# Kernel tuning notes

Hardware: AMD Instinct MI355X
Metric: run time of the kernel (lower is better)

The kernel has to match this reference:

```python
import jax, jax.numpy as jnp
import numpy as np

B = 1_000_000   # collocation points
N = 64          # layers[1]: number of tiny identity-init linear+activation layers
D = 3           # layers[0]: per-layer feature dim (rho, p, u columns)


def setup_inputs() -> dict:
    key = jax.random.key(0)
    k_x, k_w, k_cr, k_cp, k_cu = jax.random.split(key, 5)
    x = jax.random.normal(k_x, (B, D), dtype=jnp.float32)
    # Per-layer weights: identity init (as in the module) plus small noise so
    # the N layers are not all identical in the test harness.
    eye = jnp.eye(D, dtype=jnp.float32)
    W = eye[None, :, :] + 0.01 * jax.random.normal(k_w, (N, D, D), dtype=jnp.float32)
    b = jnp.zeros((N, D), dtype=jnp.float32)
    # Frozen output heads (Linear(N, 1, bias=False)), all initialized from c_initial.
    c_rho = jax.random.normal(k_cr, (1, N), dtype=jnp.float32)
    c_p = jax.random.normal(k_cp, (1, N), dtype=jnp.float32)
    c_u = jax.random.normal(k_cu, (1, N), dtype=jnp.float32)
    return {"x": x, "W": W, "b": b, "c_rho": c_rho, "c_p": c_p, "c_u": c_u}


def reference(x, W, b, c_rho, c_p, c_u):
    # Original loop: for i in range(N): u = act(Linear_i(x)); gather columns 0,1,2
    # and iteratively torch.cat them. Vectorized: one batched tiny GEMM over all
    # N layers, then slice the three channels.
    # x: [B, D]; W: [N, D, D]; b: [N, D] -> u: [B, N, D]
    u = jnp.tanh(jnp.einsum('bd,nkd->bnk', x, W) + b[None, :, :])
    u_rho = u[:, :, 0]   # [B, N]
    u_p = u[:, :, 1]
    u_u = u[:, :, 2]
    out_rho = u_rho @ c_rho.T   # [B, 1]
    out_p = u_p @ c_p.T
    out_u = u_u @ c_u.T
    return (out_rho, out_p, out_u)
```

## Files before the change

### kernel.cpp

```cpp
#include <hip/hip_runtime.h>


#define NN   64
#define RPT  4
#define BLK  256

__device__ __forceinline__ float fexp2(float x) {
#if __has_builtin(__builtin_amdgcn_exp2f)
    return __builtin_amdgcn_exp2f(x);
#else
    return exp2f(x);
#endif
}
__device__ __forceinline__ float frcp(float x) {
#if __has_builtin(__builtin_amdgcn_rcpf)
    return __builtin_amdgcn_rcpf(x);
#else
    return 1.0f / x;
#endif
}

__global__ __launch_bounds__(BLK) void fused_tanh_heads(
    const float* __restrict__ x,
    const float* __restrict__ W,
    const float* __restrict__ bias,
    const float* __restrict__ c_rho,
    const float* __restrict__ c_p,
    const float* __restrict__ c_u,
    float* __restrict__ out,
    int B)
{
    __shared__ float sc[NN * 16];
    const int t = threadIdx.x;
    #pragma unroll
    for (int k = 0; k < 4; ++k) {
        const int idx = t + BLK * k;
        const int n = idx >> 4;
        const int o = idx & 15;
        const float K = 2.8853900817779268f;
        float v;
        if (o < 9)       v = W[n * 9 + o] * K;
        else if (o < 12) v = bias[n * 3 + (o - 9)] * K;
        else if (o == 12) v = c_rho[n];
        else if (o == 13) v = c_p[n];
        else if (o == 14) v = c_u[n];
        else              v = 0.0f;
        sc[idx] = v;
    }
    __syncthreads();

    float C0 = c_rho[t & 63], C1 = c_p[t & 63], C2 = c_u[t & 63];
    #pragma unroll
    for (int o = 1; o < 64; o <<= 1) {
        C0 += __shfl_xor(C0, o);
        C1 += __shfl_xor(C1, o);
        C2 += __shfl_xor(C2, o);
    }

    const int base = blockIdx.x * (BLK * RPT) + t;

    int   rows[RPT];
    float xs[RPT][3];
    #pragma unroll
    for (int i = 0; i < RPT; ++i) {
        const int r = base + i * BLK;
        rows[i] = r;
        const bool ok = (r < B);
        xs[i][0] = ok ? x[r * 3 + 0] : 0.0f;
        xs[i][1] = ok ? x[r * 3 + 1] : 0.0f;
        xs[i][2] = ok ? x[r * 3 + 2] : 0.0f;
    }

    float acc[RPT][3];
    #pragma unroll
    for (int i = 0; i < RPT; ++i) { acc[i][0] = acc[i][1] = acc[i][2] = 0.0f; }

    const float4* q4 = (const float4*)sc;
    #pragma unroll 2
    for (int n = 0; n < NN; ++n) {
        const float4 q0 = q4[n * 4 + 0];
        const float4 q1 = q4[n * 4 + 1];
        const float4 q2 = q4[n * 4 + 2];
        const float4 q3 = q4[n * 4 + 3];
        #pragma unroll
        for (int i = 0; i < RPT; ++i) {
            const float x0 = xs[i][0], x1 = xs[i][1], x2 = xs[i][2];
            const float h0 = fmaf(x2, q0.z, fmaf(x1, q0.y, fmaf(x0, q0.x, q2.y)));
            const float h1 = fmaf(x2, q1.y, fmaf(x1, q1.x, fmaf(x0, q0.w, q2.z)));
            const float h2 = fmaf(x2, q2.x, fmaf(x1, q1.w, fmaf(x0, q1.z, q2.w)));
            const float a0 = fexp2(h0) + 1.0f;
            const float a1 = fexp2(h1) + 1.0f;
            const float a2 = fexp2(h2) + 1.0f;
            const float m  = a0 * a1;
            const float rr = frcp(m * a2);
            const float i2 = m  * rr;
            const float s  = a2 * rr;
            const float i0 = a1 * s;
            const float i1 = a0 * s;
            acc[i][0] = fmaf(i0, q3.x, acc[i][0]);
            acc[i][1] = fmaf(i1, q3.y, acc[i][1]);
            acc[i][2] = fmaf(i2, q3.z, acc[i][2]);
        }
    }

    #pragma unroll
    for (int i = 0; i < RPT; ++i) {
        const int r = rows[i];
        if (r < B) {
            out[r]         = fmaf(-2.0f, acc[i][0], C0);
            out[B + r]     = fmaf(-2.0f, acc[i][1], C1);
            out[2 * B + r] = fmaf(-2.0f, acc[i][2], C2);
        }
    }
}

extern "C" void kernel_launch(void* const* d_in, const int* in_sizes, int n_in,
                              void* d_out, int out_size, void* d_ws, size_t ws_size,
                              hipStream_t stream) {
    (void)d_ws; (void)ws_size; (void)n_in; (void)out_size;
    const float* x     = (const float*)d_in[0];
    const float* W     = (const float*)d_in[1];
    const float* bias  = (const float*)d_in[2];
    const float* c_rho = (const float*)d_in[3];
    const float* c_p   = (const float*)d_in[4];
    const float* c_u   = (const float*)d_in[5];
    float* out = (float*)d_out;

    const int B = in_sizes[0] / 3;
    const int rows_per_block = BLK * RPT;
    const int grid = (B + rows_per_block - 1) / rows_per_block;

    fused_tanh_heads<<<grid, BLK, 0, stream>>>(x, W, bias, c_rho, c_p, c_u, out, B);
}
```

Measured before the change: 126.1 us.

## Precompute parameter table in setup kernel and read it via uniform global loads

Adds a one-wave setup kernel that writes the scaled weight/bias/head table and the head sums into the workspace buffer. The main kernel drops its shared-memory staging, barrier and per-block shuffle reduction, and reads the table through wave-uniform global loads that the compiler may turn into scalar loads. Each thread now handles one row instead of four, and the grid is four times larger. The trade-off is an extra kernel launch, less per-row reuse of each table load, and possibly worse latency hiding because each thread has less independent work.

```diff
diff --git a/kernel.cpp b/kernel.cpp
--- a/kernel.cpp
+++ b/kernel.cpp
@@ -2,7 +2,6 @@
 
 
 #define NN   64
-#define RPT  4
 #define BLK  256
 
 __device__ __forceinline__ float fexp2(float x) {
@@ -20,104 +19,86 @@
 #endif
 }
 
-__global__ __launch_bounds__(BLK) void fused_tanh_heads(
-    const float* __restrict__ x,
-    const float* __restrict__ W,
-    const float* __restrict__ bias,
-    const float* __restrict__ c_rho,
-    const float* __restrict__ c_p,
-    const float* __restrict__ c_u,
-    float* __restrict__ out,
-    int B)
+__global__ __launch_bounds__(64) void setup_tab(
+    const float* __restrict__ W, const float* __restrict__ bias,
+    const float* __restrict__ c_rho, const float* __restrict__ c_p,
+    const float* __restrict__ c_u, float* __restrict__ ws)
 {
-    __shared__ float sc[NN * 16];
     const int t = threadIdx.x;
+    const float K = 2.8853900817779268f;
+    float* rec = ws + t * 16;
     #pragma unroll
-    for (int k = 0; k < 4; ++k) {
-        const int idx = t + BLK * k;
-        const int n = idx >> 4;
-        const int o = idx & 15;
-        const float K = 2.8853900817779268f;
-        float v;
-        if (o < 9)       v = W[n * 9 + o] * K;
-        else if (o < 12) v = bias[n * 3 + (o - 9)] * K;
-        else if (o == 12) v = c_rho[n];
-        else if (o == 13) v = c_p[n];
-        else if (o == 14) v = c_u[n];
-        else              v = 0.0f;
-        sc[idx] = v;
-    }
-    __syncthreads();
+    for (int j = 0; j < 9; ++j) rec[j] = W[t * 9 + j] * K;
+    #pragma unroll
+    for (int k = 0; k < 3; ++k) rec[9 + k] = bias[t * 3 + k] * K;
+    const float cr = c_rho[t], cp = c_p[t], cu = c_u[t];
+    rec[12] = cr; rec[13] = cp; rec[14] = cu; rec[15] = 0.0f;
 
-    float C0 = c_rho[t & 63], C1 = c_p[t & 63], C2 = c_u[t & 63];
+    float C0 = cr, C1 = cp, C2 = cu;
     #pragma unroll
     for (int o = 1; o < 64; o <<= 1) {
         C0 += __shfl_xor(C0, o);
         C1 += __shfl_xor(C1, o);
         C2 += __shfl_xor(C2, o);
     }
+    if (t == 0) { ws[1024] = C0; ws[1025] = C1; ws[1026] = C2; }
+}
 
-    const int base = blockIdx.x * (BLK * RPT) + t;
+__global__ __launch_bounds__(BLK) void fused_tanh_heads(
+    const float* __restrict__ x,
+    const float* __restrict__ ws,
+    float* __restrict__ out,
+    int B)
+{
+    const float C0 = ws[1024], C1 = ws[1025], C2 = ws[1026];
 
-    int   rows[RPT];
-    float xs[RPT][3];
-    #pragma unroll
-    for (int i = 0; i < RPT; ++i) {
-        const int r = base + i * BLK;
-        rows[i] = r;
-        const bool ok = (r < B);
-        xs[i][0] = ok ? x[r * 3 + 0] : 0.0f;
-        xs[i][1] = ok ? x[r * 3 + 1] : 0.0f;
-        xs[i][2] = ok ? x[r * 3 + 2] : 0.0f;
-    }
+    const int r = blockIdx.x * BLK + threadIdx.x;
+    const bool ok = (r < B);
+    const float x0 = ok ? x[r * 3 + 0] : 0.0f;
+    const float x1 = ok ? x[r * 3 + 1] : 0.0f;
+    const float x2 = ok ? x[r * 3 + 2] : 0.0f;
 
-    float acc[RPT][3];
-    #pragma unroll
-    for (int i = 0; i < RPT; ++i) { acc[i][0] = acc[i][1] = acc[i][2] = 0.0f; }
+    float acc0 = 0.0f, acc1 = 0.0f, acc2 = 0.0f;
 
-    const float4* q4 = (const float4*)sc;
-    #pragma unroll 2
+    const float4* __restrict__ q4 = (const float4*)ws;
+    #pragma unroll 4
     for (int n = 0; n < NN; ++n) {
         const float4 q0 = q4[n * 4 + 0];
         const float4 q1 = q4[n * 4 + 1];
         const float4 q2 = q4[n * 4 + 2];
         const float4 q3 = q4[n * 4 + 3];
-        #pragma unroll
-        for (int i = 0; i < RPT; ++i) {
-            const float x0 = xs[i][0], x1 = xs[i][1], x2 = xs[i][2];
-            const float h0 = fmaf(x2, q0.z, fmaf(x1, q0.y, fmaf(x0, q0.x, q2.y)));
-            const float h1 = fmaf(x2, q1.y, fmaf(x1, q1.x, fmaf(x0, q0.w, q2.z)));
-            const float h2 = fmaf(x2, q2.x, fmaf(x1, q1.w, fmaf(x0, q1.z, q2.w)));
-            const float a0 = fexp2(h0) + 1.0f;
-            const float a1 = fexp2(h1) + 1.0f;
-            const float a2 = fexp2(h2) + 1.0f;
-            const float m  = a0 * a1;
-            const float rr = frcp(m * a2);
-            const float i2 = m  * rr;
-            const float s  = a2 * rr;
-            const float i0 = a1 * s;
-            const float i1 = a0 * s;
-            acc[i][0] = fmaf(i0, q3.x, acc[i][0]);
-            acc[i][1] = fmaf(i1, q3.y, acc[i][1]);
-            acc[i][2] = fmaf(i2, q3.z, acc[i][2]);
-        }
+
+        const float h0 = fmaf(x2, q0.z, fmaf(x1, q0.y, fmaf(x0, q0.x, q2.y)));
+        const float h1 = fmaf(x2, q1.y, fmaf(x1, q1.x, fmaf(x0, q0.w, q2.z)));
+        const float h2 = fmaf(x2, q2.x, fmaf(x1, q1.w, fmaf(x0, q1.z, q2.w)));
+
+        const float a0 = fexp2(h0) + 1.0f;
+        const float a1 = fexp2(h1) + 1.0f;
+        const float a2 = fexp2(h2) + 1.0f;
+
+        const float m  = a0 * a1;
+        const float R  = frcp(m * a2);
+        const float i2 = m  * R;
+        const float s  = a2 * R;
+        const float i0 = a1 * s;
+        const float i1 = a0 * s;
+
+        acc0 = fmaf(i0, q3.x, acc0);
+        acc1 = fmaf(i1, q3.y, acc1);
+        acc2 = fmaf(i2, q3.z, acc2);
     }
 
-    #pragma unroll
-    for (int i = 0; i < RPT; ++i) {
-        const int r = rows[i];
-        if (r < B) {
-            out[r]         = fmaf(-2.0f, acc[i][0], C0);
-            out[B + r]     = fmaf(-2.0f, acc[i][1], C1);
-            out[2 * B + r] = fmaf(-2.0f, acc[i][2], C2);
-        }
+    if (ok) {
+        out[r]         = fmaf(-2.0f, acc0, C0);
+        out[B + r]     = fmaf(-2.0f, acc1, C1);
+        out[2 * B + r] = fmaf(-2.0f, acc2, C2);
     }
 }
 
 extern "C" void kernel_launch(void* const* d_in, const int* in_sizes, int n_in,
                               void* d_out, int out_size, void* d_ws, size_t ws_size,
                               hipStream_t stream) {
-    (void)d_ws; (void)ws_size; (void)n_in; (void)out_size;
+    (void)ws_size; (void)n_in; (void)out_size;
     const float* x     = (const float*)d_in[0];
     const float* W     = (const float*)d_in[1];
     const float* bias  = (const float*)d_in[2];
@@ -125,10 +106,11 @@
     const float* c_p   = (const float*)d_in[4];
     const float* c_u   = (const float*)d_in[5];
     float* out = (float*)d_out;
+    float* ws  = (float*)d_ws;
 
     const int B = in_sizes[0] / 3;
-    const int rows_per_block = BLK * RPT;
-    const int grid = (B + rows_per_block - 1) / rows_per_block;
+    const int grid = (B + BLK - 1) / BLK;
 
-    fused_tanh_heads<<<grid, BLK, 0, stream>>>(x, W, bias, c_rho, c_p, c_u, out, B);
+    setup_tab<<<1, 64, 0, stream>>>(W, bias, c_rho, c_p, c_u, ws);
+    fused_tanh_heads<<<grid, BLK, 0, stream>>>(x, ws, out, B);
 }
```

New measurement: 119.4 us. 5.3% less time.
